# Kernel optimization log

Measured on AMD Instinct MI355X. Metric: run time of the kernel, lower is better.

The kernel has to match this reference:

```python
import jax, jax.numpy as jnp
import numpy as np

def setup_inputs() -> dict:
    key = jax.random.key(0)
    ks = jax.random.split(key, 8)
    E, D_IN, D_OUT = 250000, 256, 256
    NUM_CAMS, NUM_POINTS = 500, 100000
    return {
        "edge_features": jax.random.normal(ks[0], (E, D_IN), dtype=jnp.float32),
        "cam_indices": jax.random.randint(ks[1], (E,), 0, NUM_CAMS, dtype=jnp.int64 if jax.config.jax_enable_x64 else jnp.int32),
        "point_indices": jax.random.randint(ks[2], (E,), 0, NUM_POINTS, dtype=jnp.int64 if jax.config.jax_enable_x64 else jnp.int32),
        "num_cams": NUM_CAMS,
        "num_points": NUM_POINTS,
        "W_cam": jax.random.normal(ks[3], (D_OUT, D_IN), dtype=jnp.float32) / np.sqrt(D_IN),
        "W_point": jax.random.normal(ks[4], (D_OUT, D_IN), dtype=jnp.float32) / np.sqrt(D_IN),
        "W_attn": jax.random.normal(ks[5], (1, 2 * D_OUT), dtype=jnp.float32) / np.sqrt(2 * D_OUT),
        "W_final": jax.random.normal(ks[6], (D_OUT, 2 * D_OUT), dtype=jnp.float32) / np.sqrt(2 * D_OUT),
        "b_final": jax.random.normal(ks[7], (D_OUT,), dtype=jnp.float32) * 0.01,
    }

def reference(edge_features, cam_indices, point_indices, num_cams, num_points,
              W_cam, W_point, W_attn, W_final, b_final):
    # scatter-add aggregation per camera / per point node
    cam_agg = jax.ops.segment_sum(edge_features, cam_indices, num_segments=num_cams)      # [C, d_in]
    point_agg = jax.ops.segment_sum(edge_features, point_indices, num_segments=num_points)  # [P, d_in]
    # node projections (torch Linear: y = x @ W.T)
    h_cam = cam_agg @ W_cam.T        # [C, d_out]
    h_point = point_agg @ W_point.T  # [P, d_out]
    # gather back per edge and concat
    concat = jnp.concatenate([h_cam[cam_indices], h_point[point_indices]], axis=1)  # [E, 2*d_out]
    # attention score with GLOBAL softmax over all edges (dim=0)
    e = concat @ W_attn.T                       # [E, 1]
    attn = jax.nn.softmax(e, axis=0)            # [E, 1]
    new_features = (concat @ W_final.T + b_final) * attn  # [E, d_out]
    return jax.nn.relu(new_features)
```

## Files before the change

kernel.cpp:

```cpp
#include <hip/hip_runtime.h>
#include <hip/hip_bf16.h>
#include <math.h>

#define D 256
#define NCAM 500
#define NPT 100000

__global__ void scatter_kernel(const float* __restrict__ ef,
                               const int* __restrict__ ci,
                               const int* __restrict__ pi,
                               float* __restrict__ cam_agg,
                               float* __restrict__ pt_agg, int E) {
    int e = blockIdx.x;
    if (e >= E) return;
    int c = ci[e];
    int p = pi[e];
    int f = threadIdx.x;
    float v = ef[(size_t)e * D + f];
    atomicAdd(&pt_agg[(size_t)p * D + f], v);
    atomicAdd(&cam_agg[(size_t)c * D + f], v);
}

__global__ void combine_weights(const float* __restrict__ Wcam,
                                const float* __restrict__ Wpt,
                                const float* __restrict__ Wattn,
                                const float* __restrict__ Wfin,
                                float* __restrict__ CcamT,
                                float* __restrict__ Cpt,
                                float* __restrict__ vcam,
                                float* __restrict__ vpt) {
    int b = blockIdx.x;
    int i = threadIdx.x;
    if (b < 256) {
        int o = b;
        float acc = 0.f;
        for (int j = 0; j < 256; j++) acc += Wfin[o * 512 + j] * Wcam[j * 256 + i];
        CcamT[i * 256 + o] = acc;
    } else if (b < 512) {
        int o = b - 256;
        float acc = 0.f;
        for (int j = 0; j < 256; j++) acc += Wfin[o * 512 + 256 + j] * Wpt[j * 256 + i];
        Cpt[o * 256 + i] = acc;
    } else if (b == 512) {
        float acc = 0.f;
        for (int j = 0; j < 256; j++) acc += Wattn[j] * Wcam[j * 256 + i];
        vcam[i] = acc;
    } else {
        float acc = 0.f;
        for (int j = 0; j < 256; j++) acc += Wattn[256 + j] * Wpt[j * 256 + i];
        vpt[i] = acc;
    }
}

__global__ void cam_proj(const float* __restrict__ cam_agg,
                         const float* __restrict__ CcamT,
                         const float* __restrict__ vcam,
                         float* __restrict__ gcam,
                         float* __restrict__ acam) {
    __shared__ float row[256];
    __shared__ float red[256];
    int c = blockIdx.x;
    int t = threadIdx.x;
    row[t] = cam_agg[(size_t)c * 256 + t];
    __syncthreads();
    float acc = 0.f;
    for (int i = 0; i < 256; i++) acc += row[i] * CcamT[i * 256 + t];
    gcam[(size_t)c * 256 + t] = acc;
    red[t] = row[t] * vcam[t];
    __syncthreads();
    for (int s = 128; s > 0; s >>= 1) {
        if (t < s) red[t] += red[t + s];
        __syncthreads();
    }
    if (t == 0) acam[c] = red[0];
}

#define BM 64
#define BN 64
#define BK 32
__global__ __launch_bounds__(256) void gemm_pt(const float* __restrict__ A,
                                               const float* __restrict__ Bmat,
                                               float* __restrict__ Cout, int M) {
    __shared__ float As[BK][BM + 4];
    __shared__ float Bs[BK][BN + 4];
    int m0 = blockIdx.x * BM;
    int n0 = blockIdx.y * BN;
    int tid = threadIdx.x;
    int arow = tid >> 2;
    int acol = (tid & 3) * 8;
    int tm = (tid >> 4) << 2;
    int tn = (tid & 15) << 2;
    float acc[4][4] = {};
    for (int k0 = 0; k0 < 256; k0 += BK) {
        const float* aptr = A + (size_t)(m0 + arow) * 256 + k0 + acol;
        float4 av0 = *(const float4*)aptr;
        float4 av1 = *(const float4*)(aptr + 4);
        const float* bptr = Bmat + (size_t)(n0 + arow) * 256 + k0 + acol;
        float4 bv0 = *(const float4*)bptr;
        float4 bv1 = *(const float4*)(bptr + 4);
        As[acol + 0][arow] = av0.x; As[acol + 1][arow] = av0.y;
        As[acol + 2][arow] = av0.z; As[acol + 3][arow] = av0.w;
        As[acol + 4][arow] = av1.x; As[acol + 5][arow] = av1.y;
        As[acol + 6][arow] = av1.z; As[acol + 7][arow] = av1.w;
        Bs[acol + 0][arow] = bv0.x; Bs[acol + 1][arow] = bv0.y;
        Bs[acol + 2][arow] = bv0.z; Bs[acol + 3][arow] = bv0.w;
        Bs[acol + 4][arow] = bv1.x; Bs[acol + 5][arow] = bv1.y;
        Bs[acol + 6][arow] = bv1.z; Bs[acol + 7][arow] = bv1.w;
        __syncthreads();
#pragma unroll
        for (int k = 0; k < BK; k++) {
            float4 a = *(const float4*)&As[k][tm];
            float4 b = *(const float4*)&Bs[k][tn];
            acc[0][0] += a.x * b.x; acc[0][1] += a.x * b.y; acc[0][2] += a.x * b.z; acc[0][3] += a.x * b.w;
            acc[1][0] += a.y * b.x; acc[1][1] += a.y * b.y; acc[1][2] += a.y * b.z; acc[1][3] += a.y * b.w;
            acc[2][0] += a.z * b.x; acc[2][1] += a.z * b.y; acc[2][2] += a.z * b.z; acc[2][3] += a.z * b.w;
            acc[3][0] += a.w * b.x; acc[3][1] += a.w * b.y; acc[3][2] += a.w * b.z; acc[3][3] += a.w * b.w;
        }
        __syncthreads();
    }
#pragma unroll
    for (int i = 0; i < 4; i++) {
        int m = m0 + tm + i;
        if (m < M) {
            float4 v = make_float4(acc[i][0], acc[i][1], acc[i][2], acc[i][3]);
            *(float4*)&Cout[(size_t)m * 256 + n0 + tn] = v;
        }
    }
}

__global__ void apt_kernel(const float* __restrict__ A,
                           const float* __restrict__ vpt,
                           float* __restrict__ apt, int M) {
    __shared__ float vs[256];
    vs[threadIdx.x] = vpt[threadIdx.x];
    __syncthreads();
    int wave = threadIdx.x >> 6;
    int lane = threadIdx.x & 63;
    int row = blockIdx.x * 4 + wave;
    if (row >= M) return;
    const float* a = A + (size_t)row * 256;
    float acc = 0.f;
    for (int i = lane; i < 256; i += 64) acc += a[i] * vs[i];
    for (int off = 32; off > 0; off >>= 1) acc += __shfl_down(acc, off);
    if (lane == 0) apt[row] = acc;
}

__device__ __forceinline__ unsigned float_key(float f) {
    unsigned b = __float_as_uint(f);
    return (b & 0x80000000u) ? ~b : (b | 0x80000000u);
}
__device__ __forceinline__ float key_float(unsigned k) {
    return __uint_as_float((k & 0x80000000u) ? (k & 0x7FFFFFFFu) : ~k);
}

__global__ void e_max_kernel(const int* __restrict__ ci, const int* __restrict__ pi,
                             const float* __restrict__ acam, const float* __restrict__ apt,
                             float* __restrict__ ebuf, unsigned* __restrict__ maxkey, int E) {
    int i = blockIdx.x * 256 + threadIdx.x;
    float e = -INFINITY;
    if (i < E) {
        e = acam[ci[i]] + apt[pi[i]];
        ebuf[i] = e;
    }
    __shared__ float red[256];
    int t = threadIdx.x;
    red[t] = e;
    __syncthreads();
    for (int s = 128; s > 0; s >>= 1) {
        if (t < s) red[t] = fmaxf(red[t], red[t + s]);
        __syncthreads();
    }
    if (t == 0) atomicMax(maxkey, float_key(red[0]));
}

__global__ void sumexp_kernel(float* __restrict__ ebuf,
                              const unsigned* __restrict__ maxkey,
                              float* __restrict__ sumexp, int E) {
    int i = blockIdx.x * 256 + threadIdx.x;
    float mx = key_float(*maxkey);
    float p = 0.f;
    if (i < E) {
        p = expf(ebuf[i] - mx);
        ebuf[i] = p;
    }
    __shared__ float red[256];
    int t = threadIdx.x;
    red[t] = p;
    __syncthreads();
    for (int s = 128; s > 0; s >>= 1) {
        if (t < s) red[t] += red[t + s];
        __syncthreads();
    }
    if (t == 0) atomicAdd(sumexp, red[0]);
}

__global__ void out_kernel(const int* __restrict__ ci, const int* __restrict__ pi,
                           const float* __restrict__ gcam, const float* __restrict__ gpt,
                           const float* __restrict__ bfin, const float* __restrict__ ebuf,
                           const float* __restrict__ sumexp, float* __restrict__ out, int E) {
    int e = blockIdx.x;
    int t = threadIdx.x;
    float scale = ebuf[e] / (*sumexp);
    int c = ci[e];
    int p = pi[e];
    float v = (gcam[(size_t)c * 256 + t] + gpt[(size_t)p * 256 + t] + bfin[t]) * scale;
    out[(size_t)e * 256 + t] = fmaxf(v, 0.f);
}

extern "C" void kernel_launch(void* const* d_in, const int* in_sizes, int n_in,
                              void* d_out, int out_size, void* d_ws, size_t ws_size,
                              hipStream_t stream) {
    const float* ef    = (const float*)d_in[0];
    const int*   ci    = (const int*)d_in[1];
    const int*   pi    = (const int*)d_in[2];
    const float* Wcam  = (const float*)d_in[5];
    const float* Wpt   = (const float*)d_in[6];
    const float* Wattn = (const float*)d_in[7];
    const float* Wfin  = (const float*)d_in[8];
    const float* bfin  = (const float*)d_in[9];
    float* out = (float*)d_out;
    int E = in_sizes[0] / D;

    float* ws = (float*)d_ws;
    float* cam_agg = ws;
    float* pt_agg  = cam_agg + (size_t)NCAM * D;
    float* CcamT   = pt_agg + (size_t)NPT * D;
    float* Cpt     = CcamT + 65536;
    float* vcam    = Cpt + 65536;
    float* vpt     = vcam + 256;
    float* gcam    = vpt + 256;
    float* acam    = gcam + (size_t)NCAM * D;
    float* gpt     = acam + 512;
    float* apt     = gpt + (size_t)NPT * D;
    float* ebuf    = apt + NPT;
    unsigned* maxkey = (unsigned*)(ebuf + E);
    float* sumexp  = (float*)(maxkey + 1);

    hipMemsetAsync(cam_agg, 0, (size_t)(NCAM + NPT) * D * sizeof(float), stream);
    hipMemsetAsync(maxkey, 0, 2 * sizeof(unsigned), stream);

    scatter_kernel<<<E, 256, 0, stream>>>(ef, ci, pi, cam_agg, pt_agg, E);
    combine_weights<<<514, 256, 0, stream>>>(Wcam, Wpt, Wattn, Wfin, CcamT, Cpt, vcam, vpt);
    cam_proj<<<NCAM, 256, 0, stream>>>(cam_agg, CcamT, vcam, gcam, acam);
    dim3 g4((NPT + BM - 1) / BM, 256 / BN);
    gemm_pt<<<g4, 256, 0, stream>>>(pt_agg, Cpt, gpt, NPT);
    apt_kernel<<<(NPT + 3) / 4, 256, 0, stream>>>(pt_agg, vpt, apt, NPT);
    int eb = (E + 255) / 256;
    e_max_kernel<<<eb, 256, 0, stream>>>(ci, pi, acam, apt, ebuf, maxkey, E);
    sumexp_kernel<<<eb, 256, 0, stream>>>(ebuf, maxkey, sumexp, E);
    out_kernel<<<E, 256, 0, stream>>>(ci, pi, gcam, gpt, bfin, ebuf, sumexp, out, E);
}
```

Baseline: 1.167 ms.

## Replace atomic scatter with CSR-sorted segment gather and enlarge point GEMM tiles

Replaces the per-element atomicAdd scatter with a counting-sort pipeline: a histogram, prefix scans, and a fill step build per-point and per-camera edge lists. Dedicated gather kernels then sum the rows without atomics, and camera sums are split into 8 partials that cam_proj reduces. This targets the heavy float atomic contention on the 500 camera rows, at the cost of extra passes and a single-block serial scan over 100k points. The point GEMM also moves to 128x128 tiles with 8x8 per-thread accumulators, which raises register pressure.

Measured after the change: 1.397 ms. +19.7%, slower.

```diff
diff --git a/kernel.cpp b/kernel.cpp
--- a/kernel.cpp
+++ b/kernel.cpp
@@ -6,19 +6,98 @@
 #define NCAM 500
 #define NPT 100000
 
-__global__ void scatter_kernel(const float* __restrict__ ef,
-                               const int* __restrict__ ci,
-                               const int* __restrict__ pi,
-                               float* __restrict__ cam_agg,
-                               float* __restrict__ pt_agg, int E) {
-    int e = blockIdx.x;
-    if (e >= E) return;
-    int c = ci[e];
-    int p = pi[e];
-    int f = threadIdx.x;
-    float v = ef[(size_t)e * D + f];
-    atomicAdd(&pt_agg[(size_t)p * D + f], v);
-    atomicAdd(&cam_agg[(size_t)c * D + f], v);
+
+__global__ void hist_kernel(const int* __restrict__ ci, const int* __restrict__ pi,
+                            int* __restrict__ cam_cnt, int* __restrict__ pt_cnt, int E) {
+    int i = blockIdx.x * 256 + threadIdx.x;
+    if (i < E) {
+        atomicAdd(&pt_cnt[pi[i]], 1);
+        atomicAdd(&cam_cnt[ci[i]], 1);
+    }
+}
+
+__global__ void scan_cam_kernel(const int* __restrict__ cnt,
+                                int* __restrict__ start, int* __restrict__ cur) {
+    __shared__ int s[512];
+    int t = threadIdx.x;
+    int v0 = (t < NCAM) ? cnt[t] : 0;
+    s[t] = v0;
+    __syncthreads();
+    for (int off = 1; off < 512; off <<= 1) {
+        int v = (t >= off) ? s[t - off] : 0;
+        __syncthreads();
+        s[t] += v;
+        __syncthreads();
+    }
+    if (t < NCAM) {
+        int ex = s[t] - v0;
+        start[t] = ex;
+        cur[t] = ex;
+    }
+}
+
+__global__ void scan_pt_kernel(const int* __restrict__ cnt,
+                               int* __restrict__ start, int* __restrict__ cur) {
+    __shared__ int s[1024];
+    const int CH = (NPT + 1023) / 1024;
+    int t = threadIdx.x;
+    int lo = t * CH;
+    int hi = lo + CH; if (hi > NPT) hi = NPT;
+    int sum = 0;
+    for (int i = lo; i < hi; i++) sum += cnt[i];
+    s[t] = sum;
+    __syncthreads();
+    for (int off = 1; off < 1024; off <<= 1) {
+        int v = (t >= off) ? s[t - off] : 0;
+        __syncthreads();
+        s[t] += v;
+        __syncthreads();
+    }
+    int run = s[t] - sum;
+    for (int i = lo; i < hi; i++) {
+        start[i] = run;
+        cur[i] = run;
+        run += cnt[i];
+    }
+}
+
+__global__ void fill_kernel(const int* __restrict__ ci, const int* __restrict__ pi,
+                            int* __restrict__ cam_cur, int* __restrict__ pt_cur,
+                            int* __restrict__ cam_list, int* __restrict__ pt_list, int E) {
+    int i = blockIdx.x * 256 + threadIdx.x;
+    if (i < E) {
+        pt_list[atomicAdd(&pt_cur[pi[i]], 1)] = i;
+        cam_list[atomicAdd(&cam_cur[ci[i]], 1)] = i;
+    }
+}
+
+__global__ void pt_agg_kernel(const float* __restrict__ ef,
+                              const int* __restrict__ pt_start, const int* __restrict__ pt_cnt,
+                              const int* __restrict__ pt_list, float* __restrict__ pt_agg) {
+    int p = blockIdx.x;
+    int t = threadIdx.x;
+    int s0 = pt_start[p], n = pt_cnt[p];
+    float acc = 0.f;
+    for (int j = 0; j < n; j++) {
+        int e = pt_list[s0 + j];
+        acc += ef[(size_t)e * D + t];
+    }
+    pt_agg[(size_t)p * D + t] = acc;
+}
+
+__global__ void cam_agg_kernel(const float* __restrict__ ef,
+                               const int* __restrict__ cam_start, const int* __restrict__ cam_cnt,
+                               const int* __restrict__ cam_list, float* __restrict__ cam_part) {
+    int c = blockIdx.x >> 3;
+    int part = blockIdx.x & 7;
+    int t = threadIdx.x;
+    int s0 = cam_start[c], n = cam_cnt[c];
+    float acc = 0.f;
+    for (int j = part; j < n; j += 8) {
+        int e = cam_list[s0 + j];
+        acc += ef[(size_t)e * D + t];
+    }
+    cam_part[(size_t)blockIdx.x * D + t] = acc;
 }
 
 __global__ void combine_weights(const float* __restrict__ Wcam,
@@ -52,7 +131,7 @@
     }
 }
 
-__global__ void cam_proj(const float* __restrict__ cam_agg,
+__global__ void cam_proj(const float* __restrict__ cam_part,
                          const float* __restrict__ CcamT,
                          const float* __restrict__ vcam,
                          float* __restrict__ gcam,
@@ -61,12 +140,15 @@
     __shared__ float red[256];
     int c = blockIdx.x;
     int t = threadIdx.x;
-    row[t] = cam_agg[(size_t)c * 256 + t];
+    float r = 0.f;
+#pragma unroll
+    for (int k = 0; k < 8; k++) r += cam_part[(size_t)(c * 8 + k) * 256 + t];
+    row[t] = r;
     __syncthreads();
     float acc = 0.f;
     for (int i = 0; i < 256; i++) acc += row[i] * CcamT[i * 256 + t];
     gcam[(size_t)c * 256 + t] = acc;
-    red[t] = row[t] * vcam[t];
+    red[t] = r * vcam[t];
     __syncthreads();
     for (int s = 128; s > 0; s >>= 1) {
         if (t < s) red[t] += red[t + s];
@@ -75,8 +157,8 @@
     if (t == 0) acam[c] = red[0];
 }
 
-#define BM 64
-#define BN 64
+#define BM 128
+#define BN 128
 #define BK 32
 __global__ __launch_bounds__(256) void gemm_pt(const float* __restrict__ A,
                                                const float* __restrict__ Bmat,
@@ -86,44 +168,59 @@
     int m0 = blockIdx.x * BM;
     int n0 = blockIdx.y * BN;
     int tid = threadIdx.x;
-    int arow = tid >> 2;
-    int acol = (tid & 3) * 8;
-    int tm = (tid >> 4) << 2;
-    int tn = (tid & 15) << 2;
-    float acc[4][4] = {};
+    int lrow = tid >> 1;
+    int lcol = (tid & 1) * 16;
+    int tm = (tid >> 4) << 3;
+    int tn = (tid & 15) << 3;
+    float acc[8][8] = {};
+    int arow = m0 + lrow; if (arow > M - 1) arow = M - 1;
     for (int k0 = 0; k0 < 256; k0 += BK) {
-        const float* aptr = A + (size_t)(m0 + arow) * 256 + k0 + acol;
-        float4 av0 = *(const float4*)aptr;
-        float4 av1 = *(const float4*)(aptr + 4);
-        const float* bptr = Bmat + (size_t)(n0 + arow) * 256 + k0 + acol;
-        float4 bv0 = *(const float4*)bptr;
-        float4 bv1 = *(const float4*)(bptr + 4);
-        As[acol + 0][arow] = av0.x; As[acol + 1][arow] = av0.y;
-        As[acol + 2][arow] = av0.z; As[acol + 3][arow] = av0.w;
-        As[acol + 4][arow] = av1.x; As[acol + 5][arow] = av1.y;
-        As[acol + 6][arow] = av1.z; As[acol + 7][arow] = av1.w;
-        Bs[acol + 0][arow] = bv0.x; Bs[acol + 1][arow] = bv0.y;
-        Bs[acol + 2][arow] = bv0.z; Bs[acol + 3][arow] = bv0.w;
-        Bs[acol + 4][arow] = bv1.x; Bs[acol + 5][arow] = bv1.y;
-        Bs[acol + 6][arow] = bv1.z; Bs[acol + 7][arow] = bv1.w;
-        __syncthreads();
+        const float* ap = A + (size_t)arow * 256 + k0 + lcol;
+        const float* bp = Bmat + (size_t)(n0 + lrow) * 256 + k0 + lcol;
+        float4 a0 = *(const float4*)ap;
+        float4 a1 = *(const float4*)(ap + 4);
+        float4 a2 = *(const float4*)(ap + 8);
+        float4 a3 = *(const float4*)(ap + 12);
+        float4 b0 = *(const float4*)bp;
+        float4 b1 = *(const float4*)(bp + 4);
+        float4 b2 = *(const float4*)(bp + 8);
+        float4 b3 = *(const float4*)(bp + 12);
+        As[lcol + 0][lrow] = a0.x;  As[lcol + 1][lrow] = a0.y;
+        As[lcol + 2][lrow] = a0.z;  As[lcol + 3][lrow] = a0.w;
+        As[lcol + 4][lrow] = a1.x;  As[lcol + 5][lrow] = a1.y;
+        As[lcol + 6][lrow] = a1.z;  As[lcol + 7][lrow] = a1.w;
+        As[lcol + 8][lrow] = a2.x;  As[lcol + 9][lrow] = a2.y;
+        As[lcol + 10][lrow] = a2.z; As[lcol + 11][lrow] = a2.w;
+        As[lcol + 12][lrow] = a3.x; As[lcol + 13][lrow] = a3.y;
+        As[lcol + 14][lrow] = a3.z; As[lcol + 15][lrow] = a3.w;
+        Bs[lcol + 0][lrow] = b0.x;  Bs[lcol + 1][lrow] = b0.y;
+        Bs[lcol + 2][lrow] = b0.z;  Bs[lcol + 3][lrow] = b0.w;
+        Bs[lcol + 4][lrow] = b1.x;  Bs[lcol + 5][lrow] = b1.y;
+        Bs[lcol + 6][lrow] = b1.z;  Bs[lcol + 7][lrow] = b1.w;
+        Bs[lcol + 8][lrow] = b2.x;  Bs[lcol + 9][lrow] = b2.y;
+        Bs[lcol + 10][lrow] = b2.z; Bs[lcol + 11][lrow] = b2.w;
+        Bs[lcol + 12][lrow] = b3.x; Bs[lcol + 13][lrow] = b3.y;
+        Bs[lcol + 14][lrow] = b3.z; Bs[lcol + 15][lrow] = b3.w;
+        __syncthreads();
+        for (int k = 0; k < BK; k++) {
+            float a[8], b[8];
+            *(float4*)&a[0] = *(const float4*)&As[k][tm];
+            *(float4*)&a[4] = *(const float4*)&As[k][tm + 4];
+            *(float4*)&b[0] = *(const float4*)&Bs[k][tn];
+            *(float4*)&b[4] = *(const float4*)&Bs[k][tn + 4];
 #pragma unroll
-        for (int k = 0; k < BK; k++) {
-            float4 a = *(const float4*)&As[k][tm];
-            float4 b = *(const float4*)&Bs[k][tn];
-            acc[0][0] += a.x * b.x; acc[0][1] += a.x * b.y; acc[0][2] += a.x * b.z; acc[0][3] += a.x * b.w;
-            acc[1][0] += a.y * b.x; acc[1][1] += a.y * b.y; acc[1][2] += a.y * b.z; acc[1][3] += a.y * b.w;
-            acc[2][0] += a.z * b.x; acc[2][1] += a.z * b.y; acc[2][2] += a.z * b.z; acc[2][3] += a.z * b.w;
-            acc[3][0] += a.w * b.x; acc[3][1] += a.w * b.y; acc[3][2] += a.w * b.z; acc[3][3] += a.w * b.w;
+            for (int i = 0; i < 8; i++)
+#pragma unroll
+                for (int j = 0; j < 8; j++) acc[i][j] += a[i] * b[j];
         }
         __syncthreads();
     }
 #pragma unroll
-    for (int i = 0; i < 4; i++) {
+    for (int i = 0; i < 8; i++) {
         int m = m0 + tm + i;
         if (m < M) {
-            float4 v = make_float4(acc[i][0], acc[i][1], acc[i][2], acc[i][3]);
-            *(float4*)&Cout[(size_t)m * 256 + n0 + tn] = v;
+            *(float4*)&Cout[(size_t)m * 256 + n0 + tn] = make_float4(acc[i][0], acc[i][1], acc[i][2], acc[i][3]);
+            *(float4*)&Cout[(size_t)m * 256 + n0 + tn + 4] = make_float4(acc[i][4], acc[i][5], acc[i][6], acc[i][7]);
         }
     }
 }
@@ -222,30 +319,46 @@
     int E = in_sizes[0] / D;
 
     float* ws = (float*)d_ws;
-    float* cam_agg = ws;
-    float* pt_agg  = cam_agg + (size_t)NCAM * D;
-    float* CcamT   = pt_agg + (size_t)NPT * D;
-    float* Cpt     = CcamT + 65536;
-    float* vcam    = Cpt + 65536;
-    float* vpt     = vcam + 256;
-    float* gcam    = vpt + 256;
-    float* acam    = gcam + (size_t)NCAM * D;
-    float* gpt     = acam + 512;
-    float* apt     = gpt + (size_t)NPT * D;
-    float* ebuf    = apt + NPT;
+    float* pt_agg   = ws;
+    float* CcamT    = pt_agg + (size_t)NPT * D;
+    float* Cpt      = CcamT + 65536;
+    float* vcam     = Cpt + 65536;
+    float* vpt      = vcam + 256;
+    float* gcam     = vpt + 256;
+    float* acam     = gcam + (size_t)NCAM * D;
+    float* cam_part = acam + 512;
+    float* gpt      = cam_part + (size_t)NCAM * 8 * D;
+    float* apt      = gpt + (size_t)NPT * D;
+    float* ebuf     = apt + NPT;
     unsigned* maxkey = (unsigned*)(ebuf + E);
-    float* sumexp  = (float*)(maxkey + 1);
-
-    hipMemsetAsync(cam_agg, 0, (size_t)(NCAM + NPT) * D * sizeof(float), stream);
+    float* sumexp   = (float*)(maxkey + 1);
+
+    int* sb        = (int*)gpt;
+    int* pt_cnt    = sb;
+    int* cam_cnt   = pt_cnt + NPT;
+    int* pt_start  = cam_cnt + 512;
+    int* cam_start = pt_start + NPT;
+    int* pt_cur    = cam_start + 512;
+    int* cam_cur   = pt_cur + NPT;
+    int* pt_list   = cam_cur + 512;
+    int* cam_list  = pt_list + E;
+
+    hipMemsetAsync(pt_cnt, 0, (size_t)(NPT + 512) * sizeof(int), stream);
     hipMemsetAsync(maxkey, 0, 2 * sizeof(unsigned), stream);
 
-    scatter_kernel<<<E, 256, 0, stream>>>(ef, ci, pi, cam_agg, pt_agg, E);
+    int eb = (E + 255) / 256;
+    hist_kernel<<<eb, 256, 0, stream>>>(ci, pi, cam_cnt, pt_cnt, E);
+    scan_cam_kernel<<<1, 512, 0, stream>>>(cam_cnt, cam_start, cam_cur);
+    scan_pt_kernel<<<1, 1024, 0, stream>>>(pt_cnt, pt_start, pt_cur);
+    fill_kernel<<<eb, 256, 0, stream>>>(ci, pi, cam_cur, pt_cur, cam_list, pt_list, E);
+    pt_agg_kernel<<<NPT, 256, 0, stream>>>(ef, pt_start, pt_cnt, pt_list, pt_agg);
+    cam_agg_kernel<<<NCAM * 8, 256, 0, stream>>>(ef, cam_start, cam_cnt, cam_list, cam_part);
+
     combine_weights<<<514, 256, 0, stream>>>(Wcam, Wpt, Wattn, Wfin, CcamT, Cpt, vcam, vpt);
-    cam_proj<<<NCAM, 256, 0, stream>>>(cam_agg, CcamT, vcam, gcam, acam);
+    cam_proj<<<NCAM, 256, 0, stream>>>(cam_part, CcamT, vcam, gcam, acam);
     dim3 g4((NPT + BM - 1) / BM, 256 / BN);
     gemm_pt<<<g4, 256, 0, stream>>>(pt_agg, Cpt, gpt, NPT);
     apt_kernel<<<(NPT + 3) / 4, 256, 0, stream>>>(pt_agg, vpt, apt, NPT);
-    int eb = (E + 255) / 256;
     e_max_kernel<<<eb, 256, 0, stream>>>(ci, pi, acam, apt, ebuf, maxkey, E);
     sumexp_kernel<<<eb, 256, 0, stream>>>(ebuf, maxkey, sumexp, E);
     out_kernel<<<E, 256, 0, stream>>>(ci, pi, gcam, gpt, bfin, ebuf, sumexp, out, E);
```
